# Kernel optimization log

Measured on AMD Instinct MI355X. Metric: run time of the kernel, lower is better.

Reference implementation:

```python
import jax, jax.numpy as jnp
import numpy as np

B, H, S, D = 2, 16, 2048, 64

def setup_inputs() -> dict:
    key = jax.random.key(0)
    kq, kk, kv = jax.random.split(key, 3)
    q = jax.random.normal(kq, (B, H, S, D), dtype=jnp.float32)
    k = jax.random.normal(kk, (B, H, S, D), dtype=jnp.float32)
    v = jax.random.normal(kv, (B, H, S, D), dtype=jnp.float32)
    return {"q": q, "k": k, "v": v}

def reference(q, k, v):
    # Faithful to the source: raw exp (no max-subtraction), no 1/sqrt(d) scaling.
    scores = jnp.einsum("bhsd,bhtd->bhst", q, k)          # [B,H,S,S]
    scores_exp = jnp.exp(scores)
    probs = scores_exp / jnp.sum(scores_exp, axis=-1, keepdims=True)
    return jnp.einsum("bhst,bhtd->bhsd", probs, v)         # [B,H,S,D]
```

## Files before the change

kernel.cpp:

```cpp
#include <hip/hip_runtime.h>


#define LOG2E 1.44269504088896340736f

typedef _Float16 half8 __attribute__((ext_vector_type(8)));
typedef __fp16 fp16x2 __attribute__((ext_vector_type(2)));
typedef float f32x16 __attribute__((ext_vector_type(16)));

#define BH   32
#define SEQ  2048
#define DIM  64
#define QBLK 64
#define KVB  32
#define NIT  (SEQ / (2 * KVB))

union SMem {
  struct { _Float16 K[2][KVB * DIM]; _Float16 Vt[2][DIM * KVB]; } s;
  struct { float ob[2][32 * 64]; float m[2][64]; float l[2][64]; } c;
};

static __device__ __forceinline__ unsigned pk2(float a, float b) {
  fp16x2 h = __builtin_amdgcn_cvt_pkrtz(a, b);
  return __builtin_bit_cast(unsigned, h);
}

__launch_bounds__(256, 4)
__global__ void attn_fwd(const float* __restrict__ Q, const float* __restrict__ K,
                         const float* __restrict__ V, float* __restrict__ O) {
  __shared__ __align__(16) SMem sm;

  const int tid  = threadIdx.x;
  const int lane = tid & 63;
  const int wave = tid >> 6;
  const int wq   = wave & 1;
  const int wk   = wave >> 1;
  const int hi   = lane >> 5;
  const int lq   = lane & 31;

  const int bid  = blockIdx.x;
  const int xcd  = bid & 7;
  const int slot = bid >> 3;
  const int bh   = xcd + 8 * (slot >> 5);
  const int qt   = slot & 31;

  const size_t base = (size_t)bh * SEQ * DIM;
  const int qrow = qt * QBLK + wq * 32 + lq;
  const float* qp = Q + base + (size_t)qrow * DIM;

  half8 qfrag[4];
#pragma unroll
  for (int c = 0; c < 4; ++c) {
    float4 a = *(const float4*)(qp + 16 * c + 8 * hi);
    float4 b = *(const float4*)(qp + 16 * c + 8 * hi + 4);
    union { unsigned u[4]; half8 v; } h;
    h.u[0] = pk2(a.x, a.y); h.u[1] = pk2(a.z, a.w);
    h.u[2] = pk2(b.x, b.y); h.u[3] = pk2(b.z, b.w);
    qfrag[c] = h.v;
  }

  f32x16 oacc0 = {};
  f32x16 oacc1 = {};
  float m = -1e30f, lsum = 0.f;

  float4 kreg[2][2];
  float  vreg[2][8];
  const int kr  = tid >> 3;
  const int kd  = (tid & 7) * 8;
  const int vd  = tid & 63;
  const int vk0 = (tid >> 6) * 8;
  const float* kbp = K + base;
  const float* vbp = V + base;

  auto LOADT = [&](int it) {
#pragma unroll
    for (int p = 0; p < 2; ++p) {
      const int t = 2 * it + p;
      const float* kp = kbp + (size_t)(t * KVB + kr) * DIM + kd;
      kreg[p][0] = *(const float4*)(kp);
      kreg[p][1] = *(const float4*)(kp + 4);
      const float* vp = vbp + (size_t)(t * KVB + vk0) * DIM + vd;
#pragma unroll
      for (int j = 0; j < 8; ++j) vreg[p][j] = vp[j * DIM];
    }
  };

  auto STORET = [&]() {
#pragma unroll
    for (int p = 0; p < 2; ++p) {
      union { unsigned u[4]; half8 v; } h;
      h.u[0] = pk2(kreg[p][0].x, kreg[p][0].y);
      h.u[1] = pk2(kreg[p][0].z, kreg[p][0].w);
      h.u[2] = pk2(kreg[p][1].x, kreg[p][1].y);
      h.u[3] = pk2(kreg[p][1].z, kreg[p][1].w);
      const int idx = (kr * DIM + kd) ^ ((kr & 7) << 3);
      *(half8*)&sm.s.K[p][idx] = h.v;
      union { unsigned u[4]; half8 v; } g;
      g.u[0] = pk2(vreg[p][0], vreg[p][1]);
      g.u[1] = pk2(vreg[p][2], vreg[p][3]);
      g.u[2] = pk2(vreg[p][4], vreg[p][5]);
      g.u[3] = pk2(vreg[p][6], vreg[p][7]);
      const int vidx = (vd * KVB + vk0) ^ ((vd & 7) << 3);
      *(half8*)&sm.s.Vt[p][vidx] = g.v;
    }
  };

  LOADT(0);
  for (int it = 0; it < NIT; ++it) {
    __syncthreads();
    STORET();
    if (it + 1 < NIT) LOADT(it + 1);
    __syncthreads();

    const _Float16* Kt = sm.s.K[wk];
    const _Float16* Vt = sm.s.Vt[wk];

    const int ksw = (lq & 7) << 3;
    f32x16 sacc = {};
#pragma unroll
    for (int c = 0; c < 4; ++c) {
      half8 a = *(const half8*)&Kt[(lq * DIM + c * 16 + hi * 8) ^ ksw];
      sacc = __builtin_amdgcn_mfma_f32_32x32x16_f16(a, qfrag[c], sacc, 0, 0, 0);
    }
    float s[16];
#pragma unroll
    for (int i = 0; i < 16; ++i) s[i] = sacc[i];

    float tmax = s[0];
#pragma unroll
    for (int i = 1; i < 16; ++i) tmax = fmaxf(tmax, s[i]);
    tmax = fmaxf(tmax, __shfl_xor(tmax, 32));
    if (__any(tmax > m + 8.f)) {
      const float mn = fmaxf(m, tmax);
      const float corr = __builtin_amdgcn_exp2f((m - mn) * LOG2E);
      m = mn;
      lsum *= corr;
#pragma unroll
      for (int i = 0; i < 16; ++i) { oacc0[i] *= corr; oacc1[i] *= corr; }
    }
    float p[16];
    float ts = 0.f;
#pragma unroll
    for (int i = 0; i < 16; ++i) {
      p[i] = __builtin_amdgcn_exp2f((s[i] - m) * LOG2E);
      ts += p[i];
    }
    ts += __shfl_xor(ts, 32);
    lsum += ts;

    unsigned w[8], ow[8];
#pragma unroll
    for (int i = 0; i < 8; ++i) w[i] = pk2(p[2 * i], p[2 * i + 1]);
#pragma unroll
    for (int i = 0; i < 8; ++i) ow[i] = (unsigned)__shfl_xor((int)w[i], 32);

    union { unsigned u[4]; half8 v; } pf0, pf1;
    if (hi == 0) {
      pf0.u[0] = w[0];  pf0.u[1] = w[1];  pf0.u[2] = ow[0]; pf0.u[3] = ow[1];
      pf1.u[0] = w[4];  pf1.u[1] = w[5];  pf1.u[2] = ow[4]; pf1.u[3] = ow[5];
    } else {
      pf0.u[0] = ow[2]; pf0.u[1] = ow[3]; pf0.u[2] = w[2];  pf0.u[3] = w[3];
      pf1.u[0] = ow[6]; pf1.u[1] = ow[7]; pf1.u[2] = w[6];  pf1.u[3] = w[7];
    }

    const int d0 = lq, d1 = 32 + lq;
    const int sz0 = (d0 & 7) << 3, sz1 = (d1 & 7) << 3;
    {
      half8 a = *(const half8*)&Vt[(d0 * KVB + 0 + hi * 8) ^ sz0];
      oacc0 = __builtin_amdgcn_mfma_f32_32x32x16_f16(a, pf0.v, oacc0, 0, 0, 0);
    }
    {
      half8 a = *(const half8*)&Vt[(d1 * KVB + 0 + hi * 8) ^ sz1];
      oacc1 = __builtin_amdgcn_mfma_f32_32x32x16_f16(a, pf0.v, oacc1, 0, 0, 0);
    }
    {
      half8 a = *(const half8*)&Vt[(d0 * KVB + 16 + hi * 8) ^ sz0];
      oacc0 = __builtin_amdgcn_mfma_f32_32x32x16_f16(a, pf1.v, oacc0, 0, 0, 0);
    }
    {
      half8 a = *(const half8*)&Vt[(d1 * KVB + 16 + hi * 8) ^ sz1];
      oacc1 = __builtin_amdgcn_mfma_f32_32x32x16_f16(a, pf1.v, oacc1, 0, 0, 0);
    }
  }

  __syncthreads();
  if (wk == 1) {
#pragma unroll
    for (int r = 0; r < 16; ++r) {
      sm.c.ob[wq][r * 64 + lane]        = oacc0[r];
      sm.c.ob[wq][(16 + r) * 64 + lane] = oacc1[r];
    }
    sm.c.m[wq][lane] = m;
    sm.c.l[wq][lane] = lsum;
  }
  __syncthreads();
  if (wk == 0) {
    const float mb = sm.c.m[wq][lane];
    const float lb = sm.c.l[wq][lane];
    const float mx = fmaxf(m, mb);
    const float ca = __builtin_amdgcn_exp2f((m - mx) * LOG2E);
    const float cb = __builtin_amdgcn_exp2f((mb - mx) * LOG2E);
    const float inv = 1.0f / (lsum * ca + lb * cb);

    float* op = O + base + (size_t)qrow * DIM;
#pragma unroll
    for (int g = 0; g < 4; ++g) {
      float4 r0, r1;
      r0.x = (oacc0[4 * g + 0] * ca + sm.c.ob[wq][(4 * g + 0) * 64 + lane] * cb) * inv;
      r0.y = (oacc0[4 * g + 1] * ca + sm.c.ob[wq][(4 * g + 1) * 64 + lane] * cb) * inv;
      r0.z = (oacc0[4 * g + 2] * ca + sm.c.ob[wq][(4 * g + 2) * 64 + lane] * cb) * inv;
      r0.w = (oacc0[4 * g + 3] * ca + sm.c.ob[wq][(4 * g + 3) * 64 + lane] * cb) * inv;
      r1.x = (oacc1[4 * g + 0] * ca + sm.c.ob[wq][(16 + 4 * g + 0) * 64 + lane] * cb) * inv;
      r1.y = (oacc1[4 * g + 1] * ca + sm.c.ob[wq][(16 + 4 * g + 1) * 64 + lane] * cb) * inv;
      r1.z = (oacc1[4 * g + 2] * ca + sm.c.ob[wq][(16 + 4 * g + 2) * 64 + lane] * cb) * inv;
      r1.w = (oacc1[4 * g + 3] * ca + sm.c.ob[wq][(16 + 4 * g + 3) * 64 + lane] * cb) * inv;
      *(float4*)(op + 8 * g + 4 * hi) = r0;
      *(float4*)(op + 32 + 8 * g + 4 * hi) = r1;
    }
  }
}

extern "C" void kernel_launch(void* const* d_in, const int* in_sizes, int n_in,
                              void* d_out, int out_size, void* d_ws, size_t ws_size,
                              hipStream_t stream) {
  const float* q = (const float*)d_in[0];
  const float* k = (const float*)d_in[1];
  const float* v = (const float*)d_in[2];
  float* o = (float*)d_out;
  attn_fwd<<<BH * (SEQ / QBLK), 256, 0, stream>>>(q, k, v, o);
}
```

Baseline: 76.77 us.

## Double per-wave query rows to reuse K/V fragments across two MFMA sets

Each wave now processes two 32-row query sets (QBLK 128), so every K and V fragment loaded from LDS feeds two MFMAs. This halves the K/V global loads, the fp16 conversions and the LDS traffic per query row, and the independent softmax chains give the scheduler more to interleave. The change also adds s_setprio around the MFMA sections and reworks the P-fragment lane exchange to need four shuffles per set instead of eight. In exchange the grid shrinks to 512 blocks, register pressure roughly doubles (launch bounds lowered to 2 blocks per SIMD), and the combine shared memory grows.

```diff
diff --git a/kernel.cpp b/kernel.cpp
--- a/kernel.cpp
+++ b/kernel.cpp
@@ -10,13 +10,13 @@
 #define BH   32
 #define SEQ  2048
 #define DIM  64
-#define QBLK 64
+#define QBLK 128
 #define KVB  32
 #define NIT  (SEQ / (2 * KVB))
 
 union SMem {
   struct { _Float16 K[2][KVB * DIM]; _Float16 Vt[2][DIM * KVB]; } s;
-  struct { float ob[2][32 * 64]; float m[2][64]; float l[2][64]; } c;
+  struct { float ob[2][2][2][16 * 64]; float ml[2][2][2][64]; } c;
 };
 
 static __device__ __forceinline__ unsigned pk2(float a, float b) {
@@ -24,7 +24,14 @@
   return __builtin_bit_cast(unsigned, h);
 }
 
-__launch_bounds__(256, 4)
+static __device__ __forceinline__ float xmax32(float x) {
+  return fmaxf(x, __shfl_xor(x, 32));
+}
+static __device__ __forceinline__ float xsum32(float x) {
+  return x + __shfl_xor(x, 32);
+}
+
+__launch_bounds__(256, 2)
 __global__ void attn_fwd(const float* __restrict__ Q, const float* __restrict__ K,
                          const float* __restrict__ V, float* __restrict__ O) {
   __shared__ __align__(16) SMem sm;
@@ -36,31 +43,37 @@
   const int wk   = wave >> 1;
   const int hi   = lane >> 5;
   const int lq   = lane & 31;
+  const bool hb  = (hi != 0);
 
   const int bid  = blockIdx.x;
   const int xcd  = bid & 7;
   const int slot = bid >> 3;
-  const int bh   = xcd + 8 * (slot >> 5);
-  const int qt   = slot & 31;
+  const int bh   = xcd + 8 * (slot >> 4);
+  const int qt   = slot & 15;
 
   const size_t base = (size_t)bh * SEQ * DIM;
-  const int qrow = qt * QBLK + wq * 32 + lq;
-  const float* qp = Q + base + (size_t)qrow * DIM;
-
-  half8 qfrag[4];
+  const int qr0 = qt * QBLK + wq * 64 + lq;
+  const float* qpA = Q + base + (size_t)qr0 * DIM;
+  const float* qpB = qpA + 32 * DIM;
+
+  half8 qfA[4], qfB[4];
 #pragma unroll
   for (int c = 0; c < 4; ++c) {
-    float4 a = *(const float4*)(qp + 16 * c + 8 * hi);
-    float4 b = *(const float4*)(qp + 16 * c + 8 * hi + 4);
+    float4 a0 = *(const float4*)(qpA + 16 * c + 8 * hi);
+    float4 a1 = *(const float4*)(qpA + 16 * c + 8 * hi + 4);
     union { unsigned u[4]; half8 v; } h;
-    h.u[0] = pk2(a.x, a.y); h.u[1] = pk2(a.z, a.w);
-    h.u[2] = pk2(b.x, b.y); h.u[3] = pk2(b.z, b.w);
-    qfrag[c] = h.v;
-  }
-
-  f32x16 oacc0 = {};
-  f32x16 oacc1 = {};
-  float m = -1e30f, lsum = 0.f;
+    h.u[0] = pk2(a0.x, a0.y); h.u[1] = pk2(a0.z, a0.w);
+    h.u[2] = pk2(a1.x, a1.y); h.u[3] = pk2(a1.z, a1.w);
+    qfA[c] = h.v;
+    float4 b0 = *(const float4*)(qpB + 16 * c + 8 * hi);
+    float4 b1 = *(const float4*)(qpB + 16 * c + 8 * hi + 4);
+    h.u[0] = pk2(b0.x, b0.y); h.u[1] = pk2(b0.z, b0.w);
+    h.u[2] = pk2(b1.x, b1.y); h.u[3] = pk2(b1.z, b1.w);
+    qfB[c] = h.v;
+  }
+
+  f32x16 oA0 = {}, oA1 = {}, oB0 = {}, oB1 = {};
+  float mA = -1e30f, lA = 0.f, mB = -1e30f, lB = 0.f;
 
   float4 kreg[2][2];
   float  vreg[2][8];
@@ -104,6 +117,51 @@
     }
   };
 
+  auto softmax_set = [&](const f32x16& s, float& m, float& l,
+                         f32x16& o0, f32x16& o1, half8& pv0, half8& pv1) {
+    float x0 = fmaxf(fmaxf(s[0], s[1]), fmaxf(s[2], s[3]));
+    float x1 = fmaxf(fmaxf(s[4], s[5]), fmaxf(s[6], s[7]));
+    float x2 = fmaxf(fmaxf(s[8], s[9]), fmaxf(s[10], s[11]));
+    float x3 = fmaxf(fmaxf(s[12], s[13]), fmaxf(s[14], s[15]));
+    float t = xmax32(fmaxf(fmaxf(x0, x1), fmaxf(x2, x3)));
+    if (__any(t > m + 8.f)) {
+      const float mn = fmaxf(m, t);
+      const float corr = __builtin_amdgcn_exp2f((m - mn) * LOG2E);
+      m = mn; l *= corr;
+#pragma unroll
+      for (int i = 0; i < 16; ++i) { o0[i] *= corr; o1[i] *= corr; }
+    }
+    const float nml2 = -m * LOG2E;
+    float p[16];
+#pragma unroll
+    for (int i = 0; i < 16; ++i)
+      p[i] = __builtin_amdgcn_exp2f(__builtin_fmaf(s[i], LOG2E, nml2));
+    float t0 = (p[0] + p[1]) + (p[2] + p[3]);
+    float t1 = (p[4] + p[5]) + (p[6] + p[7]);
+    float t2 = (p[8] + p[9]) + (p[10] + p[11]);
+    float t3 = (p[12] + p[13]) + (p[14] + p[15]);
+    l += xsum32((t0 + t1) + (t2 + t3));
+
+    unsigned w[8];
+#pragma unroll
+    for (int i = 0; i < 8; ++i) w[i] = pk2(p[2 * i], p[2 * i + 1]);
+    unsigned y0 = hb ? w[0] : w[2];  unsigned r0 = (unsigned)__shfl_xor((int)y0, 32);
+    unsigned y1 = hb ? w[1] : w[3];  unsigned r1 = (unsigned)__shfl_xor((int)y1, 32);
+    unsigned y2 = hb ? w[4] : w[6];  unsigned r2 = (unsigned)__shfl_xor((int)y2, 32);
+    unsigned y3 = hb ? w[5] : w[7];  unsigned r3 = (unsigned)__shfl_xor((int)y3, 32);
+    union { unsigned u[4]; half8 v; } f;
+    f.u[0] = hb ? r0 : w[0];
+    f.u[1] = hb ? r1 : w[1];
+    f.u[2] = hb ? w[2] : r0;
+    f.u[3] = hb ? w[3] : r1;
+    pv0 = f.v;
+    f.u[0] = hb ? r2 : w[4];
+    f.u[1] = hb ? r3 : w[5];
+    f.u[2] = hb ? w[6] : r2;
+    f.u[3] = hb ? w[7] : r3;
+    pv1 = f.v;
+  };
+
   LOADT(0);
   for (int it = 0; it < NIT; ++it) {
     __syncthreads();
@@ -115,107 +173,86 @@
     const _Float16* Vt = sm.s.Vt[wk];
 
     const int ksw = (lq & 7) << 3;
-    f32x16 sacc = {};
+    f32x16 sA = {}, sB = {};
+    __builtin_amdgcn_s_setprio(1);
 #pragma unroll
     for (int c = 0; c < 4; ++c) {
       half8 a = *(const half8*)&Kt[(lq * DIM + c * 16 + hi * 8) ^ ksw];
-      sacc = __builtin_amdgcn_mfma_f32_32x32x16_f16(a, qfrag[c], sacc, 0, 0, 0);
-    }
-    float s[16];
-#pragma unroll
-    for (int i = 0; i < 16; ++i) s[i] = sacc[i];
-
-    float tmax = s[0];
-#pragma unroll
-    for (int i = 1; i < 16; ++i) tmax = fmaxf(tmax, s[i]);
-    tmax = fmaxf(tmax, __shfl_xor(tmax, 32));
-    if (__any(tmax > m + 8.f)) {
-      const float mn = fmaxf(m, tmax);
-      const float corr = __builtin_amdgcn_exp2f((m - mn) * LOG2E);
-      m = mn;
-      lsum *= corr;
-#pragma unroll
-      for (int i = 0; i < 16; ++i) { oacc0[i] *= corr; oacc1[i] *= corr; }
-    }
-    float p[16];
-    float ts = 0.f;
-#pragma unroll
-    for (int i = 0; i < 16; ++i) {
-      p[i] = __builtin_amdgcn_exp2f((s[i] - m) * LOG2E);
-      ts += p[i];
-    }
-    ts += __shfl_xor(ts, 32);
-    lsum += ts;
-
-    unsigned w[8], ow[8];
-#pragma unroll
-    for (int i = 0; i < 8; ++i) w[i] = pk2(p[2 * i], p[2 * i + 1]);
-#pragma unroll
-    for (int i = 0; i < 8; ++i) ow[i] = (unsigned)__shfl_xor((int)w[i], 32);
-
-    union { unsigned u[4]; half8 v; } pf0, pf1;
-    if (hi == 0) {
-      pf0.u[0] = w[0];  pf0.u[1] = w[1];  pf0.u[2] = ow[0]; pf0.u[3] = ow[1];
-      pf1.u[0] = w[4];  pf1.u[1] = w[5];  pf1.u[2] = ow[4]; pf1.u[3] = ow[5];
-    } else {
-      pf0.u[0] = ow[2]; pf0.u[1] = ow[3]; pf0.u[2] = w[2];  pf0.u[3] = w[3];
-      pf1.u[0] = ow[6]; pf1.u[1] = ow[7]; pf1.u[2] = w[6];  pf1.u[3] = w[7];
-    }
+      sA = __builtin_amdgcn_mfma_f32_32x32x16_f16(a, qfA[c], sA, 0, 0, 0);
+      sB = __builtin_amdgcn_mfma_f32_32x32x16_f16(a, qfB[c], sB, 0, 0, 0);
+    }
+    __builtin_amdgcn_s_setprio(0);
+
+    half8 pA0, pA1, pB0, pB1;
+    softmax_set(sA, mA, lA, oA0, oA1, pA0, pA1);
+    softmax_set(sB, mB, lB, oB0, oB1, pB0, pB1);
 
     const int d0 = lq, d1 = 32 + lq;
     const int sz0 = (d0 & 7) << 3, sz1 = (d1 & 7) << 3;
+    __builtin_amdgcn_s_setprio(1);
     {
       half8 a = *(const half8*)&Vt[(d0 * KVB + 0 + hi * 8) ^ sz0];
-      oacc0 = __builtin_amdgcn_mfma_f32_32x32x16_f16(a, pf0.v, oacc0, 0, 0, 0);
+      oA0 = __builtin_amdgcn_mfma_f32_32x32x16_f16(a, pA0, oA0, 0, 0, 0);
+      oB0 = __builtin_amdgcn_mfma_f32_32x32x16_f16(a, pB0, oB0, 0, 0, 0);
     }
     {
       half8 a = *(const half8*)&Vt[(d1 * KVB + 0 + hi * 8) ^ sz1];
-      oacc1 = __builtin_amdgcn_mfma_f32_32x32x16_f16(a, pf0.v, oacc1, 0, 0, 0);
+      oA1 = __builtin_amdgcn_mfma_f32_32x32x16_f16(a, pA0, oA1, 0, 0, 0);
+      oB1 = __builtin_amdgcn_mfma_f32_32x32x16_f16(a, pB0, oB1, 0, 0, 0);
     }
     {
       half8 a = *(const half8*)&Vt[(d0 * KVB + 16 + hi * 8) ^ sz0];
-      oacc0 = __builtin_amdgcn_mfma_f32_32x32x16_f16(a, pf1.v, oacc0, 0, 0, 0);
+      oA0 = __builtin_amdgcn_mfma_f32_32x32x16_f16(a, pA1, oA0, 0, 0, 0);
+      oB0 = __builtin_amdgcn_mfma_f32_32x32x16_f16(a, pB1, oB0, 0, 0, 0);
     }
     {
       half8 a = *(const half8*)&Vt[(d1 * KVB + 16 + hi * 8) ^ sz1];
-      oacc1 = __builtin_amdgcn_mfma_f32_32x32x16_f16(a, pf1.v, oacc1, 0, 0, 0);
-    }
+      oA1 = __builtin_amdgcn_mfma_f32_32x32x16_f16(a, pA1, oA1, 0, 0, 0);
+      oB1 = __builtin_amdgcn_mfma_f32_32x32x16_f16(a, pB1, oB1, 0, 0, 0);
+    }
+    __builtin_amdgcn_s_setprio(0);
   }
 
   __syncthreads();
   if (wk == 1) {
 #pragma unroll
     for (int r = 0; r < 16; ++r) {
-      sm.c.ob[wq][r * 64 + lane]        = oacc0[r];
-      sm.c.ob[wq][(16 + r) * 64 + lane] = oacc1[r];
-    }
-    sm.c.m[wq][lane] = m;
-    sm.c.l[wq][lane] = lsum;
+      sm.c.ob[wq][0][0][r * 64 + lane] = oA0[r];
+      sm.c.ob[wq][0][1][r * 64 + lane] = oA1[r];
+      sm.c.ob[wq][1][0][r * 64 + lane] = oB0[r];
+      sm.c.ob[wq][1][1][r * 64 + lane] = oB1[r];
+    }
+    sm.c.ml[wq][0][0][lane] = mA; sm.c.ml[wq][0][1][lane] = lA;
+    sm.c.ml[wq][1][0][lane] = mB; sm.c.ml[wq][1][1][lane] = lB;
   }
   __syncthreads();
   if (wk == 0) {
-    const float mb = sm.c.m[wq][lane];
-    const float lb = sm.c.l[wq][lane];
-    const float mx = fmaxf(m, mb);
-    const float ca = __builtin_amdgcn_exp2f((m - mx) * LOG2E);
-    const float cb = __builtin_amdgcn_exp2f((mb - mx) * LOG2E);
-    const float inv = 1.0f / (lsum * ca + lb * cb);
-
-    float* op = O + base + (size_t)qrow * DIM;
-#pragma unroll
-    for (int g = 0; g < 4; ++g) {
-      float4 r0, r1;
-      r0.x = (oacc0[4 * g + 0] * ca + sm.c.ob[wq][(4 * g + 0) * 64 + lane] * cb) * inv;
-      r0.y = (oacc0[4 * g + 1] * ca + sm.c.ob[wq][(4 * g + 1) * 64 + lane] * cb) * inv;
-      r0.z = (oacc0[4 * g + 2] * ca + sm.c.ob[wq][(4 * g + 2) * 64 + lane] * cb) * inv;
-      r0.w = (oacc0[4 * g + 3] * ca + sm.c.ob[wq][(4 * g + 3) * 64 + lane] * cb) * inv;
-      r1.x = (oacc1[4 * g + 0] * ca + sm.c.ob[wq][(16 + 4 * g + 0) * 64 + lane] * cb) * inv;
-      r1.y = (oacc1[4 * g + 1] * ca + sm.c.ob[wq][(16 + 4 * g + 1) * 64 + lane] * cb) * inv;
-      r1.z = (oacc1[4 * g + 2] * ca + sm.c.ob[wq][(16 + 4 * g + 2) * 64 + lane] * cb) * inv;
-      r1.w = (oacc1[4 * g + 3] * ca + sm.c.ob[wq][(16 + 4 * g + 3) * 64 + lane] * cb) * inv;
-      *(float4*)(op + 8 * g + 4 * hi) = r0;
-      *(float4*)(op + 32 + 8 * g + 4 * hi) = r1;
-    }
+    auto emit = [&](int set, int qrow, const f32x16& o0, const f32x16& o1,
+                    float m, float l) {
+      const float mb = sm.c.ml[wq][set][0][lane];
+      const float lb = sm.c.ml[wq][set][1][lane];
+      const float mx = fmaxf(m, mb);
+      const float ca = __builtin_amdgcn_exp2f((m - mx) * LOG2E);
+      const float cb = __builtin_amdgcn_exp2f((mb - mx) * LOG2E);
+      const float inv = 1.0f / (l * ca + lb * cb);
+      float* op = O + base + (size_t)qrow * DIM;
+#pragma unroll
+      for (int g = 0; g < 4; ++g) {
+        float4 r0, r1;
+        r0.x = (o0[4*g+0] * ca + sm.c.ob[wq][set][0][(4*g+0)*64 + lane] * cb) * inv;
+        r0.y = (o0[4*g+1] * ca + sm.c.ob[wq][set][0][(4*g+1)*64 + lane] * cb) * inv;
+        r0.z = (o0[4*g+2] * ca + sm.c.ob[wq][set][0][(4*g+2)*64 + lane] * cb) * inv;
+        r0.w = (o0[4*g+3] * ca + sm.c.ob[wq][set][0][(4*g+3)*64 + lane] * cb) * inv;
+        r1.x = (o1[4*g+0] * ca + sm.c.ob[wq][set][1][(4*g+0)*64 + lane] * cb) * inv;
+        r1.y = (o1[4*g+1] * ca + sm.c.ob[wq][set][1][(4*g+1)*64 + lane] * cb) * inv;
+        r1.z = (o1[4*g+2] * ca + sm.c.ob[wq][set][1][(4*g+2)*64 + lane] * cb) * inv;
+        r1.w = (o1[4*g+3] * ca + sm.c.ob[wq][set][1][(4*g+3)*64 + lane] * cb) * inv;
+        *(float4*)(op + 8 * g + 4 * hi) = r0;
+        *(float4*)(op + 32 + 8 * g + 4 * hi) = r1;
+      }
+    };
+    emit(0, qr0,      oA0, oA1, mA, lA);
+    emit(1, qr0 + 32, oB0, oB1, mB, lB);
   }
 }
 
```

Result: faster. 67.35 us (-12.3%).
